# Optimization experiments

Measured on AMD Instinct MI355X. Metric: run time of the kernel, lower is better.

The kernel has to match this reference:

```python
import jax, jax.numpy as jnp
import numpy as np

NN_SIZE = 10


def batch_normals(x, k=NN_SIZE):
    """x: (B, 3, N) NCHW point cloud -> per-point normals (B, 3, N).

    kNN (including self) -> local covariance -> smallest eigenvector.
    """
    pts = jnp.transpose(x, (0, 2, 1))  # (B, N, 3)
    sq = jnp.sum(pts * pts, axis=-1)  # (B, N)
    # pairwise squared distances (B, N, N); the inner product is a big GEMM
    d2 = sq[:, :, None] + sq[:, None, :] - 2.0 * jnp.einsum('bnd,bmd->bnm', pts, pts)
    _, idx = jax.lax.top_k(-d2, k)  # (B, N, k) nearest neighbors (incl. self)
    nbrs = jax.vmap(lambda p, i: p[i])(pts, idx)  # (B, N, k, 3)
    centered = nbrs - jnp.mean(nbrs, axis=2, keepdims=True)
    cov = jnp.einsum('bnki,bnkj->bnij', centered, centered) / k  # (B, N, 3, 3)
    _, vecs = jnp.linalg.eigh(cov)  # eigenvalues ascending
    normal = vecs[..., :, 0]  # eigenvector of smallest eigenvalue, (B, N, 3)
    return jnp.transpose(normal, (0, 2, 1))  # (B, 3, N)


def setup_inputs() -> dict:
    key = jax.random.key(0)
    k1, k2 = jax.random.split(key)
    pred = jax.random.normal(k1, (8, 3, 4096), dtype=jnp.float32)
    gt = jax.random.normal(k2, (8, 3, 4096), dtype=jnp.float32)
    return {"pred": pred, "gt": gt}


def reference(pred, gt):
    pred_normals = batch_normals(pred)
    gt_normals = batch_normals(gt)
    # metric = "mse"
    return jnp.mean((pred_normals - gt_normals) ** 2)
```

## Files before the change

### kernel.cpp

```cpp
#include <hip/hip_runtime.h>
#include <math.h>

#define NPTS 4096
#define KNN 10
#define CAP 48
#define TAU_SLACK 1e-4f

__device__ __forceinline__ float med3f(float a, float b, float c) {
    return __builtin_amdgcn_fmed3f(a, b, c);
}


__device__ __forceinline__ float slapy2_(float x, float y) {
    float ax = fabsf(x), ay = fabsf(y);
    float w = fmaxf(ax, ay), z = fminf(ax, ay);
    if (z == 0.f) return w;
    float t = z / w;
    return w * sqrtf(1.f + t * t);
}

__device__ __forceinline__ void slartg_(float f, float g, float* c, float* s, float* r) {
    if (g == 0.f) { *c = 1.f; *s = 0.f; *r = f; }
    else if (f == 0.f) { *c = 0.f; *s = copysignf(1.f, g); *r = fabsf(g); }
    else {
        float f1 = fabsf(f);
        float d = sqrtf(f * f + g * g);
        float rr = copysignf(d, f);
        *c = f1 / d;
        *s = g / rr;
        *r = rr;
    }
}

__device__ void slaev2_(float a, float b, float c,
                        float* rt1, float* rt2, float* cs1, float* sn1) {
    float sm = a + c;
    float df = a - c;
    float adf = fabsf(df);
    float tb = b + b;
    float ab = fabsf(tb);
    float acmx, acmn;
    if (fabsf(a) > fabsf(c)) { acmx = a; acmn = c; } else { acmx = c; acmn = a; }
    float rt;
    if (adf > ab)      { float t = ab / adf; rt = adf * sqrtf(1.f + t * t); }
    else if (adf < ab) { float t = adf / ab; rt = ab * sqrtf(1.f + t * t); }
    else               { rt = ab * sqrtf(2.f); }
    int sgn1;
    if (sm < 0.f) {
        *rt1 = 0.5f * (sm - rt); sgn1 = -1;
        *rt2 = (acmx / *rt1) * acmn - (b / *rt1) * b;
    } else if (sm > 0.f) {
        *rt1 = 0.5f * (sm + rt); sgn1 = 1;
        *rt2 = (acmx / *rt1) * acmn - (b / *rt1) * b;
    } else {
        *rt1 = 0.5f * rt; *rt2 = -0.5f * rt; sgn1 = 1;
    }
    int sgn2;
    float cs;
    if (df >= 0.f) { cs = df + rt; sgn2 = 1; } else { cs = df - rt; sgn2 = -1; }
    float acs = fabsf(cs);
    if (acs > ab) {
        float ct = -tb / cs;
        *sn1 = 1.f / sqrtf(1.f + ct * ct);
        *cs1 = ct * (*sn1);
    } else {
        if (ab == 0.f) { *cs1 = 1.f; *sn1 = 0.f; }
        else {
            float tn = -cs / tb;
            *cs1 = 1.f / sqrtf(1.f + tn * tn);
            *sn1 = tn * (*cs1);
        }
    }
    if (sgn1 == sgn2) { float tn = *cs1; *cs1 = -(*sn1); *sn1 = tn; }
}

__device__ void steqr3_(float* d, float* e, float Z[3][3]) {
    const float eps    = 5.9604644775390625e-8f;
    const float eps2   = eps * eps;
    const float safmin = 1.17549435e-38f;
    const int n = 3, nm1 = 2;
    const int nmaxit = 90;
    int jtot = 0, l1 = 1;
    int guard = 0;

    while (l1 <= n) {
        if (++guard > 600) break;
        if (l1 > 1) e[l1 - 2] = 0.f;
        int m = n;
        if (l1 <= nm1) {
            for (int mm = l1; mm <= nm1; ++mm) {
                float tst = fabsf(e[mm - 1]);
                if (tst == 0.f) { m = mm; break; }
                if (tst <= (sqrtf(fabsf(d[mm - 1])) * sqrtf(fabsf(d[mm]))) * eps) {
                    e[mm - 1] = 0.f; m = mm; break;
                }
            }
        }
        int l = l1, lsv = l1, lend = m, lendsv = m;
        l1 = m + 1;
        if (lend == l) continue;
        float anorm = 0.f;
        for (int i = l; i <= lend; i++) anorm = fmaxf(anorm, fabsf(d[i - 1]));
        for (int i = l; i <= lend - 1; i++) anorm = fmaxf(anorm, fabsf(e[i - 1]));
        if (anorm == 0.f) continue;
        if (fabsf(d[lend - 1]) < fabsf(d[l - 1])) { lend = lsv; l = lendsv; }

        if (lend > l) {
            for (;;) {
                if (++guard > 600) return;
                int m2 = lend;
                if (l != lend) {
                    for (int mm = l; mm <= lend - 1; ++mm) {
                        float tst = e[mm - 1] * e[mm - 1];
                        if (tst <= (eps2 * fabsf(d[mm - 1])) * fabsf(d[mm]) + safmin) { m2 = mm; break; }
                    }
                }
                if (m2 < lend) e[m2 - 1] = 0.f;
                float p = d[l - 1];
                if (m2 == l) {
                    d[l - 1] = p; l = l + 1;
                    if (l <= lend) continue;
                    break;
                }
                if (m2 == l + 1) {
                    float rt1, rt2, c, s;
                    slaev2_(d[l - 1], e[l - 1], d[l], &rt1, &rt2, &c, &s);
                    for (int i = 0; i < 3; i++) {
                        float t = Z[i][l];
                        Z[i][l]     = c * t - s * Z[i][l - 1];
                        Z[i][l - 1] = s * t + c * Z[i][l - 1];
                    }
                    d[l - 1] = rt1; d[l] = rt2; e[l - 1] = 0.f;
                    l += 2;
                    if (l <= lend) continue;
                    break;
                }
                if (jtot == nmaxit) break;
                jtot++;
                float g = (d[l] - p) / (2.f * e[l - 1]);
                float r = slapy2_(g, 1.f);
                g = d[m2 - 1] - p + e[l - 1] / (g + copysignf(r, g));
                float s = 1.f, c = 1.f;
                p = 0.f;
                float csv[2], snv[2];
                for (int i = m2 - 1; i >= l; --i) {
                    float f = s * e[i - 1];
                    float b = c * e[i - 1];
                    slartg_(g, f, &c, &s, &r);
                    if (i != m2 - 1) e[i] = r;
                    g = d[i] - p;
                    r = (d[i - 1] - g) * s + 2.f * c * b;
                    p = s * r;
                    d[i] = g + p;
                    g = c * r - b;
                    csv[i - l] = c; snv[i - l] = -s;
                }
                int nrot = m2 - l;
                for (int j = nrot; j >= 1; --j) {
                    float C = csv[j - 1], S = snv[j - 1];
                    for (int i = 0; i < 3; i++) {
                        float t = Z[i][l - 1 + j];
                        Z[i][l - 1 + j] = C * t - S * Z[i][l - 2 + j];
                        Z[i][l - 2 + j] = S * t + C * Z[i][l - 2 + j];
                    }
                }
                d[l - 1] = d[l - 1] - p;
                e[l - 1] = g;
            }
        } else {
            for (;;) {
                if (++guard > 600) return;
                int m2 = lend;
                if (l != lend) {
                    for (int mm = l; mm >= lend + 1; --mm) {
                        float tst = e[mm - 2] * e[mm - 2];
                        if (tst <= (eps2 * fabsf(d[mm - 1])) * fabsf(d[mm - 2]) + safmin) { m2 = mm; break; }
                    }
                }
                if (m2 > lend) e[m2 - 2] = 0.f;
                float p = d[l - 1];
                if (m2 == l) {
                    d[l - 1] = p; l = l - 1;
                    if (l >= lend) continue;
                    break;
                }
                if (m2 == l - 1) {
                    float rt1, rt2, c, s;
                    slaev2_(d[l - 2], e[l - 2], d[l - 1], &rt1, &rt2, &c, &s);
                    for (int i = 0; i < 3; i++) {
                        float t = Z[i][l - 1];
                        Z[i][l - 1] = c * t - s * Z[i][l - 2];
                        Z[i][l - 2] = s * t + c * Z[i][l - 2];
                    }
                    d[l - 2] = rt1; d[l - 1] = rt2; e[l - 2] = 0.f;
                    l -= 2;
                    if (l >= lend) continue;
                    break;
                }
                if (jtot == nmaxit) break;
                jtot++;
                float g = (d[l - 2] - p) / (2.f * e[l - 2]);
                float r = slapy2_(g, 1.f);
                g = d[m2 - 1] - p + e[l - 2] / (g + copysignf(r, g));
                float s = 1.f, c = 1.f;
                p = 0.f;
                float csv[2], snv[2];
                for (int i = m2; i <= l - 1; ++i) {
                    float f = s * e[i - 1];
                    float b = c * e[i - 1];
                    slartg_(g, f, &c, &s, &r);
                    if (i != m2) e[i - 2] = r;
                    g = d[i - 1] - p;
                    r = (d[i] - g) * s + 2.f * c * b;
                    p = s * r;
                    d[i - 1] = g + p;
                    g = c * r - b;
                    csv[i - m2] = c; snv[i - m2] = s;
                }
                int nrot = l - m2;
                for (int j = 1; j <= nrot; ++j) {
                    float C = csv[j - 1], S = snv[j - 1];
                    for (int i = 0; i < 3; i++) {
                        float t = Z[i][m2 - 1 + j];
                        Z[i][m2 - 1 + j] = C * t - S * Z[i][m2 - 2 + j];
                        Z[i][m2 - 2 + j] = S * t + C * Z[i][m2 - 2 + j];
                    }
                }
                d[l - 1] -= p;
                e[l - 2] = g;
            }
        }
    }
    for (int ii = 2; ii <= n; ++ii) {
        int i = ii - 1, k = i;
        float p = d[i - 1];
        for (int j = ii; j <= n; ++j) {
            if (d[j - 1] < p) { k = j; p = d[j - 1]; }
        }
        if (k != i) {
            d[k - 1] = d[i - 1]; d[i - 1] = p;
            for (int r2 = 0; r2 < 3; r2++) {
                float t = Z[r2][i - 1]; Z[r2][i - 1] = Z[r2][k - 1]; Z[r2][k - 1] = t;
            }
        }
    }
}

__device__ void eig_normal3(const float xs[KNN], const float ys[KNN], const float zs[KNN],
                            float out[3]) {
    float mx = 0.f, my = 0.f, mz = 0.f;
#pragma unroll
    for (int s = 0; s < KNN; s++) { mx += xs[s]; my += ys[s]; mz += zs[s]; }
    mx /= 10.0f; my /= 10.0f; mz /= 10.0f;

    float c00 = 0.f, c10 = 0.f, c20 = 0.f, c11 = 0.f, c21 = 0.f, c22 = 0.f;
#pragma unroll
    for (int s = 0; s < KNN; s++) {
        float dx = xs[s] - mx, dy = ys[s] - my, dz = zs[s] - mz;
        c00 = fmaf(dx, dx, c00);
        c10 = fmaf(dy, dx, c10);
        c20 = fmaf(dz, dx, c20);
        c11 = fmaf(dy, dy, c11);
        c21 = fmaf(dz, dy, c21);
        c22 = fmaf(dz, dz, c22);
    }
    c00 /= 10.0f; c10 /= 10.0f; c20 /= 10.0f; c11 /= 10.0f; c21 /= 10.0f; c22 /= 10.0f;

    float alpha = c10, x2 = c20;
    float tau, v2, beta;
    float xnorm = fabsf(x2);
    if (xnorm == 0.f) { tau = 0.f; v2 = 0.f; beta = alpha; }
    else {
        beta = -copysignf(slapy2_(alpha, xnorm), alpha);
        tau = (beta - alpha) / beta;
        v2 = x2 / (alpha - beta);
    }
    float d[3], e[2];
    d[0] = c00;
    if (tau != 0.f) {
        float p0 = tau * (c11 + c21 * v2);
        float p1 = tau * (c21 + c22 * v2);
        float aw = -0.5f * tau * (p0 + p1 * v2);
        float w0 = p0 + aw;
        float w1 = p1 + aw * v2;
        d[1] = (c11 - w0) - w0;
        e[1] = (c21 - v2 * w0) - w1;
        d[2] = (c22 - v2 * w1) - w1 * v2;
        e[0] = beta;
    } else {
        d[1] = c11; d[2] = c22; e[0] = beta; e[1] = c21;
    }

    float Z[3][3] = {{1.f, 0.f, 0.f}, {0.f, 1.f, 0.f}, {0.f, 0.f, 1.f}};
    steqr3_(d, e, Z);

    float y0 = Z[0][0], y1 = Z[1][0], y2 = Z[2][0];
    if (tau != 0.f) {
        float t = tau * (y1 + v2 * y2);
        y1 = y1 - t;
        y2 = y2 - t * v2;
    }
    out[0] = y0; out[1] = y1; out[2] = y2;
}

__device__ __forceinline__ void merge_round(float* v, int off) {
    float t[KNN];
#pragma unroll
    for (int i = 0; i < KNN; i++) t[i] = fminf(v[i], __shfl_xor(v[KNN - 1 - i], off));
#define CE(a, b) { float hi = fmaxf(t[a], t[b]); float lo = fminf(t[a], t[b]); t[a] = hi; t[b] = lo; }
    CE(0, 8) CE(1, 9)
    CE(0, 4) CE(1, 5) CE(2, 6) CE(3, 7)
    CE(0, 2) CE(1, 3) CE(4, 6) CE(5, 7)
    CE(0, 1) CE(2, 3) CE(4, 5) CE(6, 7) CE(8, 9)
#undef CE
#pragma unroll
    for (int i = 0; i < KNN; i++) v[i] = t[i];
}

__device__ void exact_topk_full(const float2* sxy, const float* sz,
                                float qx, float qy, float qz, float qw,
                                float bd[KNN], int bi_[KNN]) {
#pragma unroll
    for (int s = 0; s < KNN; s++) { bd[s] = 3.4e38f; bi_[s] = 0; }
    float worst = 3.4e38f;
    int wslot = 0;
    for (int j = 0; j < NPTS; j++) {
        float2 a = sxy[j];
        float z = sz[j];
        float w = fmaf(z, z, fmaf(a.y, a.y, a.x * a.x));
        float dot = fmaf(qz, z, fmaf(qy, a.y, qx * a.x));
        float d2 = (qw + w) - 2.f * dot;
        if (d2 < worst) {
#pragma unroll
            for (int s = 0; s < KNN; s++) { if (s == wslot) { bd[s] = d2; bi_[s] = j; } }
            float wm = bd[0]; int ws = 0;
#pragma unroll
            for (int s = 1; s < KNN; s++) { if (bd[s] > wm) { wm = bd[s]; ws = s; } }
            worst = wm; wslot = ws;
        }
    }
}

__device__ void do_phase(const float* __restrict__ src, int chunk, int tid,
                         float2* sxy, float* sz, unsigned short* spairs, int* scnt,
                         float nv[3]) {
    for (int j = tid; j < NPTS; j += 512) {
        float x = src[j], y = src[NPTS + j], z = src[2 * NPTS + j];
        sxy[j] = make_float2(x, y);
        sz[j] = z;
    }
    if (tid < 128) scnt[tid] = 0;
    __syncthreads();

    int part = tid & 15;
    int qg = tid >> 4;
    int ql0 = qg * 4;
    int q0 = chunk * 128 + ql0;

    float m2x[4], m2y[4], m2z[4];
#pragma unroll
    for (int c = 0; c < 4; c++) {
        float2 a = sxy[q0 + c];
        float z = sz[q0 + c];
        m2x[c] = -2.f * a.x; m2y[c] = -2.f * a.y; m2z[c] = -2.f * z;
    }

    float v[4][KNN + 1];
#pragma unroll
    for (int c = 0; c < 4; c++) {
#pragma unroll
        for (int s = 0; s < KNN; s++) v[c][s] = INFINITY;
        v[c][KNN] = -INFINITY;
    }

#pragma unroll 2
    for (int g = 0; g < 32; g++) {
        int jb = part + 128 * g;
        float m[4] = {INFINITY, INFINITY, INFINITY, INFINITY};
#pragma unroll
        for (int u = 0; u < 8; u++) {
            int j = jb + 16 * u;
            float2 a = sxy[j];
            float z = sz[j];
            float w = fmaf(z, z, fmaf(a.y, a.y, a.x * a.x));
#pragma unroll
            for (int c = 0; c < 4; c++) {
                float key = fmaf(m2z[c], z, fmaf(m2y[c], a.y, fmaf(m2x[c], a.x, w)));
                m[c] = fminf(m[c], key);
            }
        }
#pragma unroll
        for (int c = 0; c < 4; c++)
#pragma unroll
            for (int s = 0; s < KNN; s++) v[c][s] = med3f(m[c], v[c][s], v[c][s + 1]);
    }

    float tauS[4];
#pragma unroll
    for (int c = 0; c < 4; c++) {
        merge_round(v[c], 1);
        merge_round(v[c], 2);
        merge_round(v[c], 4);
        merge_round(v[c], 8);
        tauS[c] = v[c][0] + TAU_SLACK;
    }

#pragma unroll 2
    for (int mm = 0; mm < 256; mm++) {
        int j = part + 16 * mm;
        float2 a = sxy[j];
        float z = sz[j];
        float w = fmaf(z, z, fmaf(a.y, a.y, a.x * a.x));
#pragma unroll
        for (int c = 0; c < 4; c++) {
            float key = fmaf(m2z[c], z, fmaf(m2y[c], a.y, fmaf(m2x[c], a.x, w)));
            if (key <= tauS[c]) {
                int ql = ql0 + c;
                int pos = atomicAdd(&scnt[ql], 1);
                if (pos < CAP) spairs[ql * CAP + pos] = (unsigned short)j;
            }
        }
    }
    __syncthreads();

    if (tid < 128) {
        int ql = tid;
        int qi = chunk * 128 + ql;
        float2 qa = sxy[qi];
        float qzz = sz[qi];
        float qw = fmaf(qzz, qzz, fmaf(qa.y, qa.y, qa.x * qa.x));
        int cnt = scnt[ql];

        float bd[KNN]; int bi_[KNN];
        if (cnt > CAP) {
            exact_topk_full(sxy, sz, qa.x, qa.y, qzz, qw, bd, bi_);
        } else {
#pragma unroll
            for (int s = 0; s < KNN; s++) { bd[s] = 3.4e38f; bi_[s] = 0; }
            float worst = 3.4e38f;
            int wslot = 0;
            for (int t = 0; t < cnt; t++) {
                int j = spairs[ql * CAP + t];
                float2 a = sxy[j];
                float z = sz[j];
                float w = fmaf(z, z, fmaf(a.y, a.y, a.x * a.x));
                float dot = fmaf(qzz, z, fmaf(qa.y, a.y, qa.x * a.x));
                float d2 = (qw + w) - 2.f * dot;
                if (d2 < worst) {
#pragma unroll
                    for (int s = 0; s < KNN; s++) { if (s == wslot) { bd[s] = d2; bi_[s] = j; } }
                    float wm = bd[0]; int ws = 0;
#pragma unroll
                    for (int s = 1; s < KNN; s++) { if (bd[s] > wm) { wm = bd[s]; ws = s; } }
                    worst = wm; wslot = ws;
                }
            }
        }
#pragma unroll
        for (int a = 0; a < KNN - 1; a++)
#pragma unroll
            for (int b2 = 0; b2 < KNN - 1 - a; b2++) {
                bool sw = (bd[b2] > bd[b2 + 1]) ||
                          (bd[b2] == bd[b2 + 1] && bi_[b2] > bi_[b2 + 1]);
                float d_lo = sw ? bd[b2 + 1] : bd[b2];
                float d_hi = sw ? bd[b2] : bd[b2 + 1];
                int   i_lo = sw ? bi_[b2 + 1] : bi_[b2];
                int   i_hi = sw ? bi_[b2] : bi_[b2 + 1];
                bd[b2] = d_lo; bd[b2 + 1] = d_hi; bi_[b2] = i_lo; bi_[b2 + 1] = i_hi;
            }
        float xs[KNN], ys[KNN], zs[KNN];
#pragma unroll
        for (int s = 0; s < KNN; s++) {
            int j = bi_[s];
            float2 a = sxy[j];
            xs[s] = a.x; ys[s] = a.y; zs[s] = sz[j];
        }
        eig_normal3(xs, ys, zs, nv);
    }
    __syncthreads();
}


__global__ __launch_bounds__(512, 4) void normals_kernel(const float* __restrict__ pred,
                                                         const float* __restrict__ gt,
                                                         float* __restrict__ nrm,
                                                         float* __restrict__ out) {
    __shared__ float2 sxy[NPTS];
    __shared__ float  sz[NPTS];
    __shared__ unsigned short spairs[128 * CAP];
    __shared__ int scnt[128];

    int tid = threadIdx.x;
    int bid = blockIdx.x;
    if (bid == 0 && tid == 0) out[0] = 0.f;
    int cloud = bid >> 8;
    int b = (bid >> 5) & 7;
    int chunk = bid & 31;

    const float* src = (cloud == 0 ? pred : gt) + (size_t)b * 3 * NPTS;
    float nv[3] = {0.f, 0.f, 0.f};
    do_phase(src, chunk, tid, sxy, sz, spairs, scnt, nv);

    if (tid < 128) {
        int qg2 = chunk * 128 + tid;
        float* dst = nrm + ((size_t)cloud * 8 + b) * 3 * NPTS;
        dst[0 * NPTS + qg2] = nv[0];
        dst[1 * NPTS + qg2] = nv[1];
        dst[2 * NPTS + qg2] = nv[2];
    }
}

__global__ __launch_bounds__(256) void loss_kernel(const float* __restrict__ nrm,
                                                   float* __restrict__ out) {
    const int n = 8 * 3 * NPTS;
    const float* a = nrm;
    const float* b = nrm + n;
    float acc = 0.f;
    for (int i = blockIdx.x * 256 + threadIdx.x; i < n; i += gridDim.x * 256) {
        float dd = a[i] - b[i];
        acc = fmaf(dd, dd, acc);
    }
#pragma unroll
    for (int off = 32; off > 0; off >>= 1) acc += __shfl_down(acc, off);
    __shared__ float wsum[4];
    int lane = threadIdx.x & 63, wv = threadIdx.x >> 6;
    if (lane == 0) wsum[wv] = acc;
    __syncthreads();
    if (threadIdx.x == 0) {
        float t = wsum[0] + wsum[1] + wsum[2] + wsum[3];
        atomicAdd(out, t * (1.f / (float)n));
    }
}

__global__ __launch_bounds__(512, 4) void fused_kernel(const float* __restrict__ pred,
                                                       const float* __restrict__ gt,
                                                       float* __restrict__ out) {
    __shared__ float2 sxy[NPTS];
    __shared__ float  sz[NPTS];
    __shared__ unsigned short spairs[128 * CAP];
    __shared__ int scnt[128];
    __shared__ float wsum[8];

    int tid = threadIdx.x;
    int bid = blockIdx.x;
    int b = bid >> 5;
    int chunk = bid & 31;

    const float* pbase = pred + (size_t)b * 3 * NPTS;
    const float* gbase = gt + (size_t)b * 3 * NPTS;

    float va[3] = {0.f, 0.f, 0.f}, vb[3] = {0.f, 0.f, 0.f};
    do_phase(pbase, chunk, tid, sxy, sz, spairs, scnt, va);
    do_phase(gbase, chunk, tid, sxy, sz, spairs, scnt, vb);

    float acc = 0.f;
    if (tid < 128) {
        float d0 = va[0] - vb[0], d1 = va[1] - vb[1], d2 = va[2] - vb[2];
        acc = fmaf(d2, d2, fmaf(d1, d1, d0 * d0));
    }
#pragma unroll
    for (int off = 32; off > 0; off >>= 1) acc += __shfl_down(acc, off);
    int lane = tid & 63, wv = tid >> 6;
    if (lane == 0) wsum[wv] = acc;
    __syncthreads();
    if (tid == 0) {
        float t = 0.f;
#pragma unroll
        for (int i = 0; i < 8; i++) t += wsum[i];
        atomicAdd(out, t * (1.f / (float)(8 * 3 * NPTS)));
    }
}

extern "C" void kernel_launch(void* const* d_in, const int* in_sizes, int n_in,
                              void* d_out, int out_size, void* d_ws, size_t ws_size,
                              hipStream_t stream) {
    (void)in_sizes; (void)n_in;
    const float* pred = (const float*)d_in[0];
    const float* gt   = (const float*)d_in[1];
    float* out = (float*)d_out;

    size_t need = (size_t)2 * 8 * 3 * NPTS * sizeof(float);
    if (ws_size >= need) {
        float* nrm = (float*)d_ws;
        hipLaunchKernelGGL(normals_kernel, dim3(512), dim3(512), 0, stream, pred, gt, nrm, out);
        hipLaunchKernelGGL(loss_kernel, dim3(96), dim3(256), 0, stream, nrm, out);
    } else {
        hipMemsetAsync(d_out, 0, (size_t)out_size * sizeof(float), stream);
        hipLaunchKernelGGL(fused_kernel, dim3(256), dim3(512), 0, stream, pred, gt, out);
    }
}
```

Before: 175.7 us.

## Pack points as float4 with precomputed norms and fuse loss via last-block reduction

Stores each point as a float4 (x, y, z, |p|^2) in dynamic LDS, so every distance key needs one 16-byte load and no per-pair norm recompute. The separate loss kernel is folded into the normals kernel: each block bumps an atomic counter, and the last block to finish computes the MSE over the workspace. This removes one kernel launch but adds a memset and a serial tail reduction done by a single block. LDS use rises to 64KB for points, which may reduce occupancy, and host-side attribute queries add CPU overhead on every call.

```diff
diff --git a/kernel.cpp b/kernel.cpp
--- a/kernel.cpp
+++ b/kernel.cpp
@@ -5,6 +5,8 @@
 #define KNN 10
 #define CAP 48
 #define TAU_SLACK 1e-4f
+#define NRM_N (8 * 3 * NPTS)
+#define DYN_BYTES (NPTS * 16 + 128 * CAP * 2 + 512)
 
 __device__ __forceinline__ float med3f(float a, float b, float c) {
     return __builtin_amdgcn_fmed3f(a, b, c);
@@ -317,33 +319,210 @@
     for (int i = 0; i < KNN; i++) v[i] = t[i];
 }
 
-__device__ void exact_topk_full(const float2* sxy, const float* sz,
-                                float qx, float qy, float qz, float qw,
-                                float bd[KNN], int bi_[KNN]) {
-#pragma unroll
-    for (int s = 0; s < KNN; s++) { bd[s] = 3.4e38f; bi_[s] = 0; }
-    float worst = 3.4e38f;
-    int wslot = 0;
-    for (int j = 0; j < NPTS; j++) {
-        float2 a = sxy[j];
-        float z = sz[j];
-        float w = fmaf(z, z, fmaf(a.y, a.y, a.x * a.x));
-        float dot = fmaf(qz, z, fmaf(qy, a.y, qx * a.x));
-        float d2 = (qw + w) - 2.f * dot;
-        if (d2 < worst) {
-#pragma unroll
-            for (int s = 0; s < KNN; s++) { if (s == wslot) { bd[s] = d2; bi_[s] = j; } }
-            float wm = bd[0]; int ws = 0;
-#pragma unroll
-            for (int s = 1; s < KNN; s++) { if (bd[s] > wm) { wm = bd[s]; ws = s; } }
-            worst = wm; wslot = ws;
-        }
-    }
-}
-
-__device__ void do_phase(const float* __restrict__ src, int chunk, int tid,
-                         float2* sxy, float* sz, unsigned short* spairs, int* scnt,
-                         float nv[3]) {
+__device__ void do_phase4(const float* __restrict__ src, int chunk, int tid,
+                          float4* pts, unsigned short* spairs, int* scnt,
+                          float nv[3]) {
+    for (int j = tid; j < NPTS; j += 512) {
+        float x = src[j], y = src[NPTS + j], z = src[2 * NPTS + j];
+        float w = fmaf(z, z, fmaf(y, y, x * x));
+        pts[j] = make_float4(x, y, z, w);
+    }
+    if (tid < 128) scnt[tid] = 0;
+    __syncthreads();
+
+    int part = tid & 15;
+    int qg = tid >> 4;
+    int ql0 = qg * 4;
+    int q0 = chunk * 128 + ql0;
+
+    float m2x[4], m2y[4], m2z[4];
+#pragma unroll
+    for (int c = 0; c < 4; c++) {
+        float4 p = pts[q0 + c];
+        m2x[c] = -2.f * p.x; m2y[c] = -2.f * p.y; m2z[c] = -2.f * p.z;
+    }
+
+    float v[4][KNN + 1];
+#pragma unroll
+    for (int c = 0; c < 4; c++) {
+#pragma unroll
+        for (int s = 0; s < KNN; s++) v[c][s] = INFINITY;
+        v[c][KNN] = -INFINITY;
+    }
+
+#pragma unroll 2
+    for (int g = 0; g < 32; g++) {
+        int jb = part + 128 * g;
+        float m[4] = {INFINITY, INFINITY, INFINITY, INFINITY};
+#pragma unroll
+        for (int u = 0; u < 8; u++) {
+            float4 p = pts[jb + 16 * u];
+#pragma unroll
+            for (int c = 0; c < 4; c++) {
+                float key = fmaf(m2z[c], p.z, fmaf(m2y[c], p.y, fmaf(m2x[c], p.x, p.w)));
+                m[c] = fminf(m[c], key);
+            }
+        }
+#pragma unroll
+        for (int c = 0; c < 4; c++)
+#pragma unroll
+            for (int s = 0; s < KNN; s++) v[c][s] = med3f(m[c], v[c][s], v[c][s + 1]);
+    }
+
+    float tauS[4];
+#pragma unroll
+    for (int c = 0; c < 4; c++) {
+        merge_round(v[c], 1);
+        merge_round(v[c], 2);
+        merge_round(v[c], 4);
+        merge_round(v[c], 8);
+        tauS[c] = v[c][0] + TAU_SLACK;
+    }
+
+#pragma unroll 2
+    for (int mm = 0; mm < 256; mm++) {
+        int j = part + 16 * mm;
+        float4 p = pts[j];
+#pragma unroll
+        for (int c = 0; c < 4; c++) {
+            float key = fmaf(m2z[c], p.z, fmaf(m2y[c], p.y, fmaf(m2x[c], p.x, p.w)));
+            if (key <= tauS[c]) {
+                int ql = ql0 + c;
+                int pos = atomicAdd(&scnt[ql], 1);
+                if (pos < CAP) spairs[ql * CAP + pos] = (unsigned short)j;
+            }
+        }
+    }
+    __syncthreads();
+
+    if (tid < 128) {
+        int ql = tid;
+        int qi = chunk * 128 + ql;
+        float4 q = pts[qi];
+        float qw = q.w;
+        int cnt = scnt[ql];
+
+        float bd[KNN]; int bi_[KNN];
+        if (cnt > CAP) {
+#pragma unroll
+            for (int s = 0; s < KNN; s++) { bd[s] = 3.4e38f; bi_[s] = 0; }
+            float worst = 3.4e38f;
+            int wslot = 0;
+            for (int j = 0; j < NPTS; j++) {
+                float4 p = pts[j];
+                float dot = fmaf(q.z, p.z, fmaf(q.y, p.y, q.x * p.x));
+                float d2 = (qw + p.w) - 2.f * dot;
+                if (d2 < worst) {
+#pragma unroll
+                    for (int s = 0; s < KNN; s++) { if (s == wslot) { bd[s] = d2; bi_[s] = j; } }
+                    float wm = bd[0]; int ws = 0;
+#pragma unroll
+                    for (int s = 1; s < KNN; s++) { if (bd[s] > wm) { wm = bd[s]; ws = s; } }
+                    worst = wm; wslot = ws;
+                }
+            }
+        } else {
+#pragma unroll
+            for (int s = 0; s < KNN; s++) { bd[s] = 3.4e38f; bi_[s] = 0; }
+            float worst = 3.4e38f;
+            int wslot = 0;
+            for (int t = 0; t < cnt; t++) {
+                int j = spairs[ql * CAP + t];
+                float4 p = pts[j];
+                float dot = fmaf(q.z, p.z, fmaf(q.y, p.y, q.x * p.x));
+                float d2 = (qw + p.w) - 2.f * dot;
+                if (d2 < worst) {
+#pragma unroll
+                    for (int s = 0; s < KNN; s++) { if (s == wslot) { bd[s] = d2; bi_[s] = j; } }
+                    float wm = bd[0]; int ws = 0;
+#pragma unroll
+                    for (int s = 1; s < KNN; s++) { if (bd[s] > wm) { wm = bd[s]; ws = s; } }
+                    worst = wm; wslot = ws;
+                }
+            }
+        }
+#pragma unroll
+        for (int a = 0; a < KNN - 1; a++)
+#pragma unroll
+            for (int b2 = 0; b2 < KNN - 1 - a; b2++) {
+                bool sw = (bd[b2] > bd[b2 + 1]) ||
+                          (bd[b2] == bd[b2 + 1] && bi_[b2] > bi_[b2 + 1]);
+                float d_lo = sw ? bd[b2 + 1] : bd[b2];
+                float d_hi = sw ? bd[b2] : bd[b2 + 1];
+                int   i_lo = sw ? bi_[b2 + 1] : bi_[b2];
+                int   i_hi = sw ? bi_[b2] : bi_[b2 + 1];
+                bd[b2] = d_lo; bd[b2 + 1] = d_hi; bi_[b2] = i_lo; bi_[b2 + 1] = i_hi;
+            }
+        float xs[KNN], ys[KNN], zs[KNN];
+#pragma unroll
+        for (int s = 0; s < KNN; s++) {
+            float4 p = pts[bi_[s]];
+            xs[s] = p.x; ys[s] = p.y; zs[s] = p.z;
+        }
+        eig_normal3(xs, ys, zs, nv);
+    }
+    __syncthreads();
+}
+
+__global__ __launch_bounds__(512, 4) void normals4_kernel(const float* __restrict__ pred,
+                                                          const float* __restrict__ gt,
+                                                          float* __restrict__ nrm,
+                                                          int* __restrict__ done,
+                                                          float* __restrict__ out) {
+    extern __shared__ char dynlds[];
+    float4* pts = (float4*)dynlds;
+    unsigned short* spairs = (unsigned short*)(dynlds + NPTS * 16);
+    int* scnt = (int*)(dynlds + NPTS * 16 + 128 * CAP * 2);
+    __shared__ int is_last;
+    __shared__ float wsum[8];
+
+    int tid = threadIdx.x;
+    int bid = blockIdx.x;
+    int cloud = bid >> 8;
+    int b = (bid >> 5) & 7;
+    int chunk = bid & 31;
+
+    const float* src = (cloud == 0 ? pred : gt) + (size_t)b * 3 * NPTS;
+    float nv[3] = {0.f, 0.f, 0.f};
+    do_phase4(src, chunk, tid, pts, spairs, scnt, nv);
+
+    if (tid < 128) {
+        int qg2 = chunk * 128 + tid;
+        float* dst = nrm + ((size_t)cloud * 8 + b) * 3 * NPTS;
+        dst[0 * NPTS + qg2] = nv[0];
+        dst[1 * NPTS + qg2] = nv[1];
+        dst[2 * NPTS + qg2] = nv[2];
+    }
+    __threadfence();
+    __syncthreads();
+    if (tid == 0) is_last = (atomicAdd(done, 1) == (int)gridDim.x - 1);
+    __syncthreads();
+    if (is_last) {
+        __threadfence();
+        const float* a = nrm;
+        const float* bb = nrm + NRM_N;
+        float acc = 0.f;
+        for (int i = tid; i < NRM_N; i += 512) {
+            float dd = a[i] - bb[i];
+            acc = fmaf(dd, dd, acc);
+        }
+#pragma unroll
+        for (int off = 32; off > 0; off >>= 1) acc += __shfl_down(acc, off);
+        int lane = tid & 63, wv = tid >> 6;
+        if (lane == 0) wsum[wv] = acc;
+        __syncthreads();
+        if (tid == 0) {
+            float t = 0.f;
+#pragma unroll
+            for (int i = 0; i < 8; i++) t += wsum[i];
+            out[0] = t * (1.f / (float)NRM_N);
+        }
+    }
+}
+
+__device__ void do_phase_static(const float* __restrict__ src, int chunk, int tid,
+                                float2* sxy, float* sz, unsigned short* spairs, int* scnt,
+                                float nv[3]) {
     for (int j = tid; j < NPTS; j += 512) {
         float x = src[j], y = src[NPTS + j], z = src[2 * NPTS + j];
         sxy[j] = make_float2(x, y);
@@ -432,13 +611,27 @@
         int cnt = scnt[ql];
 
         float bd[KNN]; int bi_[KNN];
+#pragma unroll
+        for (int s = 0; s < KNN; s++) { bd[s] = 3.4e38f; bi_[s] = 0; }
+        float worst = 3.4e38f;
+        int wslot = 0;
         if (cnt > CAP) {
-            exact_topk_full(sxy, sz, qa.x, qa.y, qzz, qw, bd, bi_);
+            for (int j = 0; j < NPTS; j++) {
+                float2 a = sxy[j];
+                float z = sz[j];
+                float w = fmaf(z, z, fmaf(a.y, a.y, a.x * a.x));
+                float dot = fmaf(qzz, z, fmaf(qa.y, a.y, qa.x * a.x));
+                float d2 = (qw + w) - 2.f * dot;
+                if (d2 < worst) {
+#pragma unroll
+                    for (int s = 0; s < KNN; s++) { if (s == wslot) { bd[s] = d2; bi_[s] = j; } }
+                    float wm = bd[0]; int ws = 0;
+#pragma unroll
+                    for (int s = 1; s < KNN; s++) { if (bd[s] > wm) { wm = bd[s]; ws = s; } }
+                    worst = wm; wslot = ws;
+                }
+            }
         } else {
-#pragma unroll
-            for (int s = 0; s < KNN; s++) { bd[s] = 3.4e38f; bi_[s] = 0; }
-            float worst = 3.4e38f;
-            int wslot = 0;
             for (int t = 0; t < cnt; t++) {
                 int j = spairs[ql * CAP + t];
                 float2 a = sxy[j];
@@ -480,7 +673,6 @@
     __syncthreads();
 }
 
-
 __global__ __launch_bounds__(512, 4) void normals_kernel(const float* __restrict__ pred,
                                                          const float* __restrict__ gt,
                                                          float* __restrict__ nrm,
@@ -499,7 +691,7 @@
 
     const float* src = (cloud == 0 ? pred : gt) + (size_t)b * 3 * NPTS;
     float nv[3] = {0.f, 0.f, 0.f};
-    do_phase(src, chunk, tid, sxy, sz, spairs, scnt, nv);
+    do_phase_static(src, chunk, tid, sxy, sz, spairs, scnt, nv);
 
     if (tid < 128) {
         int qg2 = chunk * 128 + tid;
@@ -512,7 +704,7 @@
 
 __global__ __launch_bounds__(256) void loss_kernel(const float* __restrict__ nrm,
                                                    float* __restrict__ out) {
-    const int n = 8 * 3 * NPTS;
+    const int n = NRM_N;
     const float* a = nrm;
     const float* b = nrm + n;
     float acc = 0.f;
@@ -532,60 +724,39 @@
     }
 }
 
-__global__ __launch_bounds__(512, 4) void fused_kernel(const float* __restrict__ pred,
-                                                       const float* __restrict__ gt,
-                                                       float* __restrict__ out) {
-    __shared__ float2 sxy[NPTS];
-    __shared__ float  sz[NPTS];
-    __shared__ unsigned short spairs[128 * CAP];
-    __shared__ int scnt[128];
-    __shared__ float wsum[8];
-
-    int tid = threadIdx.x;
-    int bid = blockIdx.x;
-    int b = bid >> 5;
-    int chunk = bid & 31;
-
-    const float* pbase = pred + (size_t)b * 3 * NPTS;
-    const float* gbase = gt + (size_t)b * 3 * NPTS;
-
-    float va[3] = {0.f, 0.f, 0.f}, vb[3] = {0.f, 0.f, 0.f};
-    do_phase(pbase, chunk, tid, sxy, sz, spairs, scnt, va);
-    do_phase(gbase, chunk, tid, sxy, sz, spairs, scnt, vb);
-
-    float acc = 0.f;
-    if (tid < 128) {
-        float d0 = va[0] - vb[0], d1 = va[1] - vb[1], d2 = va[2] - vb[2];
-        acc = fmaf(d2, d2, fmaf(d1, d1, d0 * d0));
-    }
-#pragma unroll
-    for (int off = 32; off > 0; off >>= 1) acc += __shfl_down(acc, off);
-    int lane = tid & 63, wv = tid >> 6;
-    if (lane == 0) wsum[wv] = acc;
-    __syncthreads();
-    if (tid == 0) {
-        float t = 0.f;
-#pragma unroll
-        for (int i = 0; i < 8; i++) t += wsum[i];
-        atomicAdd(out, t * (1.f / (float)(8 * 3 * NPTS)));
-    }
-}
-
 extern "C" void kernel_launch(void* const* d_in, const int* in_sizes, int n_in,
                               void* d_out, int out_size, void* d_ws, size_t ws_size,
                               hipStream_t stream) {
-    (void)in_sizes; (void)n_in;
+    (void)in_sizes; (void)n_in; (void)out_size;
     const float* pred = (const float*)d_in[0];
     const float* gt   = (const float*)d_in[1];
     float* out = (float*)d_out;
 
-    size_t need = (size_t)2 * 8 * 3 * NPTS * sizeof(float);
-    if (ws_size >= need) {
-        float* nrm = (float*)d_ws;
-        hipLaunchKernelGGL(normals_kernel, dim3(512), dim3(512), 0, stream, pred, gt, nrm, out);
+    size_t need = (size_t)2 * NRM_N * sizeof(float) + 64;
+    float* nrm = (float*)d_ws;
+    int* done = (int*)((char*)d_ws + (size_t)2 * NRM_N * sizeof(float));
+
+    int dev = 0;
+    hipGetDevice(&dev);
+    int maxShm = 0;
+    hipDeviceGetAttribute(&maxShm, hipDeviceAttributeMaxSharedMemoryPerBlock, dev);
+    hipError_t eAttr = hipFuncSetAttribute(
+        reinterpret_cast<const void*>(normals4_kernel),
+        hipFuncAttributeMaxDynamicSharedMemorySize, DYN_BYTES);
+    bool use4 = (ws_size >= need) && ((maxShm >= DYN_BYTES) || (eAttr == hipSuccess));
+
+    if (use4) {
+        hipMemsetAsync(done, 0, sizeof(int), stream);
+        hipLaunchKernelGGL(normals4_kernel, dim3(512), dim3(512), DYN_BYTES, stream,
+                           pred, gt, nrm, done, out);
+    } else if (ws_size >= need) {
+        hipLaunchKernelGGL(normals_kernel, dim3(512), dim3(512), 0, stream,
+                           pred, gt, nrm, out);
         hipLaunchKernelGGL(loss_kernel, dim3(96), dim3(256), 0, stream, nrm, out);
     } else {
-        hipMemsetAsync(d_out, 0, (size_t)out_size * sizeof(float), stream);
-        hipLaunchKernelGGL(fused_kernel, dim3(256), dim3(512), 0, stream, pred, gt, out);
-    }
-}
+        hipMemsetAsync(d_out, 0, sizeof(float), stream);
+        hipLaunchKernelGGL(normals_kernel, dim3(512), dim3(512), 0, stream,
+                           pred, gt, (float*)d_ws, out);
+        hipLaunchKernelGGL(loss_kernel, dim3(96), dim3(256), 0, stream, (float*)d_ws, out);
+    }
+}
```

New measurement: 463.8 us. +164.0%, slower.

## Pack points as float4 with precomputed norm and use 1024-thread blocks

Applied to the files above, without the earlier changes.

Point data in LDS is stored as float4 (x,y,z,|p|^2), so the squared norm is computed once at load time and each candidate needs a single 16-byte LDS read instead of a float2 plus a float load and three FMAs. The kNN phase is templated on thread count and launched with 1024 threads per block, which doubles the number of partitions scanning candidates for each query. LDS per block grows to 64KB+ and now needs a dynamic shared-memory attribute. The fused fallback path is dropped and the workspace size is no longer checked.

```diff
diff --git a/kernel.cpp b/kernel.cpp
--- a/kernel.cpp
+++ b/kernel.cpp
@@ -5,6 +5,8 @@
 #define KNN 10
 #define CAP 48
 #define TAU_SLACK 1e-4f
+#define NRM_N (8 * 3 * NPTS)
+#define DYN_BYTES (NPTS * 16 + 128 * CAP * 2 + 512)
 
 __device__ __forceinline__ float med3f(float a, float b, float c) {
     return __builtin_amdgcn_fmed3f(a, b, c);
@@ -317,52 +319,30 @@
     for (int i = 0; i < KNN; i++) v[i] = t[i];
 }
 
-__device__ void exact_topk_full(const float2* sxy, const float* sz,
-                                float qx, float qy, float qz, float qw,
-                                float bd[KNN], int bi_[KNN]) {
-#pragma unroll
-    for (int s = 0; s < KNN; s++) { bd[s] = 3.4e38f; bi_[s] = 0; }
-    float worst = 3.4e38f;
-    int wslot = 0;
-    for (int j = 0; j < NPTS; j++) {
-        float2 a = sxy[j];
-        float z = sz[j];
-        float w = fmaf(z, z, fmaf(a.y, a.y, a.x * a.x));
-        float dot = fmaf(qz, z, fmaf(qy, a.y, qx * a.x));
-        float d2 = (qw + w) - 2.f * dot;
-        if (d2 < worst) {
-#pragma unroll
-            for (int s = 0; s < KNN; s++) { if (s == wslot) { bd[s] = d2; bi_[s] = j; } }
-            float wm = bd[0]; int ws = 0;
-#pragma unroll
-            for (int s = 1; s < KNN; s++) { if (bd[s] > wm) { wm = bd[s]; ws = s; } }
-            worst = wm; wslot = ws;
-        }
-    }
-}
-
-__device__ void do_phase(const float* __restrict__ src, int chunk, int tid,
-                         float2* sxy, float* sz, unsigned short* spairs, int* scnt,
-                         float nv[3]) {
-    for (int j = tid; j < NPTS; j += 512) {
+template <int NT>
+__device__ void do_phase4(const float* __restrict__ src, int chunk, int tid,
+                          float4* pts, unsigned short* spairs, int* scnt,
+                          float nv[3]) {
+    constexpr int PARTS = NT / 32;
+    constexpr int NGRP = NPTS / (8 * PARTS);
+    for (int j = tid; j < NPTS; j += NT) {
         float x = src[j], y = src[NPTS + j], z = src[2 * NPTS + j];
-        sxy[j] = make_float2(x, y);
-        sz[j] = z;
+        float w = fmaf(z, z, fmaf(y, y, x * x));
+        pts[j] = make_float4(x, y, z, w);
     }
     if (tid < 128) scnt[tid] = 0;
     __syncthreads();
 
-    int part = tid & 15;
-    int qg = tid >> 4;
+    int part = tid & (PARTS - 1);
+    int qg = tid / PARTS;
     int ql0 = qg * 4;
     int q0 = chunk * 128 + ql0;
 
     float m2x[4], m2y[4], m2z[4];
 #pragma unroll
     for (int c = 0; c < 4; c++) {
-        float2 a = sxy[q0 + c];
-        float z = sz[q0 + c];
-        m2x[c] = -2.f * a.x; m2y[c] = -2.f * a.y; m2z[c] = -2.f * z;
+        float4 p = pts[q0 + c];
+        m2x[c] = -2.f * p.x; m2y[c] = -2.f * p.y; m2z[c] = -2.f * p.z;
     }
 
     float v[4][KNN + 1];
@@ -374,18 +354,15 @@
     }
 
 #pragma unroll 2
-    for (int g = 0; g < 32; g++) {
-        int jb = part + 128 * g;
+    for (int g = 0; g < NGRP; g++) {
+        int jb = part + (8 * PARTS) * g;
         float m[4] = {INFINITY, INFINITY, INFINITY, INFINITY};
 #pragma unroll
         for (int u = 0; u < 8; u++) {
-            int j = jb + 16 * u;
-            float2 a = sxy[j];
-            float z = sz[j];
-            float w = fmaf(z, z, fmaf(a.y, a.y, a.x * a.x));
+            float4 p = pts[jb + PARTS * u];
 #pragma unroll
             for (int c = 0; c < 4; c++) {
-                float key = fmaf(m2z[c], z, fmaf(m2y[c], a.y, fmaf(m2x[c], a.x, w)));
+                float key = fmaf(m2z[c], p.z, fmaf(m2y[c], p.y, fmaf(m2x[c], p.x, p.w)));
                 m[c] = fminf(m[c], key);
             }
         }
@@ -398,22 +375,18 @@
     float tauS[4];
 #pragma unroll
     for (int c = 0; c < 4; c++) {
-        merge_round(v[c], 1);
-        merge_round(v[c], 2);
-        merge_round(v[c], 4);
-        merge_round(v[c], 8);
+#pragma unroll
+        for (int off = 1; off < PARTS; off <<= 1) merge_round(v[c], off);
         tauS[c] = v[c][0] + TAU_SLACK;
     }
 
 #pragma unroll 2
-    for (int mm = 0; mm < 256; mm++) {
-        int j = part + 16 * mm;
-        float2 a = sxy[j];
-        float z = sz[j];
-        float w = fmaf(z, z, fmaf(a.y, a.y, a.x * a.x));
+    for (int mm = 0; mm < NPTS / PARTS; mm++) {
+        int j = part + PARTS * mm;
+        float4 p = pts[j];
 #pragma unroll
         for (int c = 0; c < 4; c++) {
-            float key = fmaf(m2z[c], z, fmaf(m2y[c], a.y, fmaf(m2x[c], a.x, w)));
+            float key = fmaf(m2z[c], p.z, fmaf(m2y[c], p.y, fmaf(m2x[c], p.x, p.w)));
             if (key <= tauS[c]) {
                 int ql = ql0 + c;
                 int pos = atomicAdd(&scnt[ql], 1);
@@ -426,26 +399,35 @@
     if (tid < 128) {
         int ql = tid;
         int qi = chunk * 128 + ql;
-        float2 qa = sxy[qi];
-        float qzz = sz[qi];
-        float qw = fmaf(qzz, qzz, fmaf(qa.y, qa.y, qa.x * qa.x));
+        float4 q = pts[qi];
+        float qw = q.w;
         int cnt = scnt[ql];
 
         float bd[KNN]; int bi_[KNN];
+#pragma unroll
+        for (int s = 0; s < KNN; s++) { bd[s] = 3.4e38f; bi_[s] = 0; }
+        float worst = 3.4e38f;
+        int wslot = 0;
         if (cnt > CAP) {
-            exact_topk_full(sxy, sz, qa.x, qa.y, qzz, qw, bd, bi_);
+            for (int j = 0; j < NPTS; j++) {
+                float4 p = pts[j];
+                float dot = fmaf(q.z, p.z, fmaf(q.y, p.y, q.x * p.x));
+                float d2 = (qw + p.w) - 2.f * dot;
+                if (d2 < worst) {
+#pragma unroll
+                    for (int s = 0; s < KNN; s++) { if (s == wslot) { bd[s] = d2; bi_[s] = j; } }
+                    float wm = bd[0]; int ws = 0;
+#pragma unroll
+                    for (int s = 1; s < KNN; s++) { if (bd[s] > wm) { wm = bd[s]; ws = s; } }
+                    worst = wm; wslot = ws;
+                }
+            }
         } else {
-#pragma unroll
-            for (int s = 0; s < KNN; s++) { bd[s] = 3.4e38f; bi_[s] = 0; }
-            float worst = 3.4e38f;
-            int wslot = 0;
             for (int t = 0; t < cnt; t++) {
                 int j = spairs[ql * CAP + t];
-                float2 a = sxy[j];
-                float z = sz[j];
-                float w = fmaf(z, z, fmaf(a.y, a.y, a.x * a.x));
-                float dot = fmaf(qzz, z, fmaf(qa.y, a.y, qa.x * a.x));
-                float d2 = (qw + w) - 2.f * dot;
+                float4 p = pts[j];
+                float dot = fmaf(q.z, p.z, fmaf(q.y, p.y, q.x * p.x));
+                float d2 = (qw + p.w) - 2.f * dot;
                 if (d2 < worst) {
 #pragma unroll
                     for (int s = 0; s < KNN; s++) { if (s == wslot) { bd[s] = d2; bi_[s] = j; } }
@@ -471,24 +453,22 @@
         float xs[KNN], ys[KNN], zs[KNN];
 #pragma unroll
         for (int s = 0; s < KNN; s++) {
-            int j = bi_[s];
-            float2 a = sxy[j];
-            xs[s] = a.x; ys[s] = a.y; zs[s] = sz[j];
+            float4 p = pts[bi_[s]];
+            xs[s] = p.x; ys[s] = p.y; zs[s] = p.z;
         }
         eig_normal3(xs, ys, zs, nv);
     }
     __syncthreads();
 }
 
-
-__global__ __launch_bounds__(512, 4) void normals_kernel(const float* __restrict__ pred,
+__global__ __launch_bounds__(1024) void normals4w_kernel(const float* __restrict__ pred,
                                                          const float* __restrict__ gt,
                                                          float* __restrict__ nrm,
                                                          float* __restrict__ out) {
-    __shared__ float2 sxy[NPTS];
-    __shared__ float  sz[NPTS];
-    __shared__ unsigned short spairs[128 * CAP];
-    __shared__ int scnt[128];
+    extern __shared__ char dynlds[];
+    float4* pts = (float4*)dynlds;
+    unsigned short* spairs = (unsigned short*)(dynlds + NPTS * 16);
+    int* scnt = (int*)(dynlds + NPTS * 16 + 128 * CAP * 2);
 
     int tid = threadIdx.x;
     int bid = blockIdx.x;
@@ -499,7 +479,7 @@
 
     const float* src = (cloud == 0 ? pred : gt) + (size_t)b * 3 * NPTS;
     float nv[3] = {0.f, 0.f, 0.f};
-    do_phase(src, chunk, tid, sxy, sz, spairs, scnt, nv);
+    do_phase4<1024>(src, chunk, tid, pts, spairs, scnt, nv);
 
     if (tid < 128) {
         int qg2 = chunk * 128 + tid;
@@ -510,9 +490,38 @@
     }
 }
 
+__global__ __launch_bounds__(512, 4) void normals4_kernel(const float* __restrict__ pred,
+                                                          const float* __restrict__ gt,
+                                                          float* __restrict__ nrm,
+                                                          float* __restrict__ out) {
+    extern __shared__ char dynlds[];
+    float4* pts = (float4*)dynlds;
+    unsigned short* spairs = (unsigned short*)(dynlds + NPTS * 16);
+    int* scnt = (int*)(dynlds + NPTS * 16 + 128 * CAP * 2);
+
+    int tid = threadIdx.x;
+    int bid = blockIdx.x;
+    if (bid == 0 && tid == 0) out[0] = 0.f;
+    int cloud = bid >> 8;
+    int b = (bid >> 5) & 7;
+    int chunk = bid & 31;
+
+    const float* src = (cloud == 0 ? pred : gt) + (size_t)b * 3 * NPTS;
+    float nv[3] = {0.f, 0.f, 0.f};
+    do_phase4<512>(src, chunk, tid, pts, spairs, scnt, nv);
+
+    if (tid < 128) {
+        int qg2 = chunk * 128 + tid;
+        float* dst = nrm + ((size_t)cloud * 8 + b) * 3 * NPTS;
+        dst[0 * NPTS + qg2] = nv[0];
+        dst[1 * NPTS + qg2] = nv[1];
+        dst[2 * NPTS + qg2] = nv[2];
+    }
+}
+
 __global__ __launch_bounds__(256) void loss_kernel(const float* __restrict__ nrm,
                                                    float* __restrict__ out) {
-    const int n = 8 * 3 * NPTS;
+    const int n = NRM_N;
     const float* a = nrm;
     const float* b = nrm + n;
     float acc = 0.f;
@@ -532,60 +541,28 @@
     }
 }
 
-__global__ __launch_bounds__(512, 4) void fused_kernel(const float* __restrict__ pred,
-                                                       const float* __restrict__ gt,
-                                                       float* __restrict__ out) {
-    __shared__ float2 sxy[NPTS];
-    __shared__ float  sz[NPTS];
-    __shared__ unsigned short spairs[128 * CAP];
-    __shared__ int scnt[128];
-    __shared__ float wsum[8];
-
-    int tid = threadIdx.x;
-    int bid = blockIdx.x;
-    int b = bid >> 5;
-    int chunk = bid & 31;
-
-    const float* pbase = pred + (size_t)b * 3 * NPTS;
-    const float* gbase = gt + (size_t)b * 3 * NPTS;
-
-    float va[3] = {0.f, 0.f, 0.f}, vb[3] = {0.f, 0.f, 0.f};
-    do_phase(pbase, chunk, tid, sxy, sz, spairs, scnt, va);
-    do_phase(gbase, chunk, tid, sxy, sz, spairs, scnt, vb);
-
-    float acc = 0.f;
-    if (tid < 128) {
-        float d0 = va[0] - vb[0], d1 = va[1] - vb[1], d2 = va[2] - vb[2];
-        acc = fmaf(d2, d2, fmaf(d1, d1, d0 * d0));
-    }
-#pragma unroll
-    for (int off = 32; off > 0; off >>= 1) acc += __shfl_down(acc, off);
-    int lane = tid & 63, wv = tid >> 6;
-    if (lane == 0) wsum[wv] = acc;
-    __syncthreads();
-    if (tid == 0) {
-        float t = 0.f;
-#pragma unroll
-        for (int i = 0; i < 8; i++) t += wsum[i];
-        atomicAdd(out, t * (1.f / (float)(8 * 3 * NPTS)));
-    }
-}
-
 extern "C" void kernel_launch(void* const* d_in, const int* in_sizes, int n_in,
                               void* d_out, int out_size, void* d_ws, size_t ws_size,
                               hipStream_t stream) {
-    (void)in_sizes; (void)n_in;
+    (void)in_sizes; (void)n_in; (void)out_size; (void)ws_size;
     const float* pred = (const float*)d_in[0];
     const float* gt   = (const float*)d_in[1];
     float* out = (float*)d_out;
-
-    size_t need = (size_t)2 * 8 * 3 * NPTS * sizeof(float);
-    if (ws_size >= need) {
-        float* nrm = (float*)d_ws;
-        hipLaunchKernelGGL(normals_kernel, dim3(512), dim3(512), 0, stream, pred, gt, nrm, out);
-        hipLaunchKernelGGL(loss_kernel, dim3(96), dim3(256), 0, stream, nrm, out);
+    float* nrm = (float*)d_ws;
+
+    hipError_t e1 = hipFuncSetAttribute(
+        reinterpret_cast<const void*>(normals4w_kernel),
+        hipFuncAttributeMaxDynamicSharedMemorySize, DYN_BYTES);
+    hipFuncSetAttribute(
+        reinterpret_cast<const void*>(normals4_kernel),
+        hipFuncAttributeMaxDynamicSharedMemorySize, DYN_BYTES);
+
+    if (e1 == hipSuccess) {
+        hipLaunchKernelGGL(normals4w_kernel, dim3(512), dim3(1024), DYN_BYTES, stream,
+                           pred, gt, nrm, out);
     } else {
-        hipMemsetAsync(d_out, 0, (size_t)out_size * sizeof(float), stream);
-        hipLaunchKernelGGL(fused_kernel, dim3(256), dim3(512), 0, stream, pred, gt, out);
-    }
-}
+        hipLaunchKernelGGL(normals4_kernel, dim3(512), dim3(512), DYN_BYTES, stream,
+                           pred, gt, nrm, out);
+    }
+    hipLaunchKernelGGL(loss_kernel, dim3(96), dim3(256), 0, stream, nrm, out);
+}
```

Measured after the change: 206.7 us. 17.6% more time.
